# Kernel tuning notes

Measured on AMD Instinct MI355X. Metric: run time of the kernel, lower is better.

Reference implementation:

```python
import jax, jax.numpy as jnp
import numpy as np

EPSILON = 0.1
NUM_ITERS = 50
D = 256


def setup_inputs() -> dict:
    key = jax.random.key(0)
    ks = jax.random.split(key, 12)
    NA, NT = 8192, 8192
    s = 1.0 / np.sqrt(D)
    return {
        "agent_embeddings": jax.random.normal(ks[0], (NA, D), jnp.float32),
        "task_embeddings": jax.random.normal(ks[1], (NT, D), jnp.float32),
        "Wq": jax.random.normal(ks[2], (D, D), jnp.float32) * s,
        "bq": jax.random.normal(ks[3], (D,), jnp.float32) * 0.01,
        "Wk": jax.random.normal(ks[4], (D, D), jnp.float32) * s,
        "bk": jax.random.normal(ks[5], (D,), jnp.float32) * 0.01,
        "W1": jax.random.normal(ks[6], (D, D // 2), jnp.float32) * s,
        "b1": jax.random.normal(ks[7], (D // 2,), jnp.float32) * 0.01,
        "W2": jax.random.normal(ks[8], (D // 2, 1), jnp.float32) * (1.0 / np.sqrt(D // 2)),
        "b2": jax.random.normal(ks[9], (1,), jnp.float32) * 0.01,
    }


def _ot_forward(agent_embeddings, task_embeddings, Wq, bq, Wk, bk, W1, b1, W2, b2):
    num_tasks = task_embeddings.shape[0]
    q = agent_embeddings @ Wq + bq  # [NA, D]
    k = task_embeddings @ Wk + bk   # [NT, D]
    q_norm = jnp.sum(q * q, axis=1, keepdims=True)          # [NA, 1]
    k_norm = jnp.sum(k * k, axis=1, keepdims=True)          # [NT, 1]
    distances = q_norm + k_norm.T - 2.0 * (q @ k.T)          # [NA, NT]
    C = -distances
    supply_logits = (jax.nn.relu(agent_embeddings @ W1 + b1) @ W2 + b2)[:, 0]
    b = jax.nn.softmax(supply_logits, axis=0)                # [NA]
    a = jnp.ones((num_tasks,), dtype=C.dtype) / num_tasks    # [NT]

    log_b = jnp.log(b + 1e-20)
    log_a = jnp.log(a + 1e-20)
    log_K = -C / EPSILON                                     # [NA, NT]

    def body(_, fg):
        f, g = fg
        f = log_b - jax.nn.logsumexp(log_K + g[None, :], axis=1)
        g = log_a - jax.nn.logsumexp(log_K + f[:, None], axis=0)
        return (f, g)

    f0 = jnp.zeros_like(b)
    g0 = jnp.zeros_like(a)
    f, g = jax.lax.fori_loop(0, NUM_ITERS, body, (f0, g0))

    T = jnp.exp(f[:, None] + log_K + g[None, :])
    T = jnp.maximum(T, 0.0)
    T = T / (jnp.sum(T) + 1e-08)
    return T


def reference(agent_embeddings, task_embeddings, Wq, bq, Wk, bk, W1, b1, W2, b2):
    return _ot_forward(agent_embeddings, task_embeddings, Wq, bq, Wk, bk, W1, b1, W2, b2)
```

## Files before the change

### kernel.cpp

```cpp
#include <hip/hip_runtime.h>
#include <math.h>

#define NR 8192
#define DIM 256
#define NBLK 512
#define CROWS 16
#define RSC 2
#define NSUB 8
#define SCALE2 14.426950408889634f

typedef unsigned short ushort_t;
typedef __attribute__((ext_vector_type(8))) short bfrag;
typedef __attribute__((ext_vector_type(4))) float facc;

__device__ __forceinline__ float fexp2(float x) {
#if __has_builtin(__builtin_amdgcn_exp2f)
    return __builtin_amdgcn_exp2f(x);
#else
    return exp2f(x);
#endif
}
__device__ __forceinline__ float flog2(float x) {
#if __has_builtin(__builtin_amdgcn_logf)
    return __builtin_amdgcn_logf(x);
#else
    return log2f(x);
#endif
}

__device__ __forceinline__ void gl2lds16(const float* gp, float* lp) {
#if __has_builtin(__builtin_amdgcn_global_load_lds)
    __builtin_amdgcn_global_load_lds(
        (const __attribute__((address_space(1))) unsigned int*)gp,
        (__attribute__((address_space(3))) unsigned int*)lp, 16, 0, 0);
#else
    *(float4*)lp = *(const float4*)gp;
#endif
}

__device__ __forceinline__ void wait_vm0()  { asm volatile("s_waitcnt vmcnt(0)" ::: "memory"); }
__device__ __forceinline__ void bar_lgkm()  { asm volatile("s_waitcnt lgkmcnt(0)\ns_barrier" ::: "memory"); }

__device__ __forceinline__ void lse_comb2(float& m, float& s, float mo, float so) {
    float nm = fmaxf(m, mo);
    s = s * fexp2(m - nm) + so * fexp2(mo - nm);
    m = nm;
}

__device__ __forceinline__ void lse_upd4(float& m, float& s,
                                         float v0, float v1, float v2, float v3) {
    float m4 = fmaxf(fmaxf(v0, v1), fmaxf(v2, v3));
    float nm = fmaxf(m, m4);
    float e = fexp2(v0 - nm) + fexp2(v1 - nm) + fexp2(v2 - nm) + fexp2(v3 - nm);
    s = fmaf(s, fexp2(m - nm), e);
    m = nm;
}

__device__ __forceinline__ void lse_upd2(float& m, float& s, float v0, float v1) {
    float m2 = fmaxf(v0, v1);
    float nm = fmaxf(m, m2);
    float e = fexp2(v0 - nm) + fexp2(v1 - nm);
    s = fmaf(s, fexp2(m - nm), e);
    m = nm;
}

__device__ __forceinline__ ushort_t f2bf(float x) {
    unsigned u = __float_as_uint(x);
    u += 0x7FFFu + ((u >> 16) & 1u);
    return (ushort_t)(u >> 16);
}
__device__ __forceinline__ float bf2f(ushort_t b) {
    return __uint_as_float(((unsigned)b) << 16);
}

__global__ void init_zero(float* __restrict__ g) {
    int t = blockIdx.x * 256 + threadIdx.x;
    if (t < NR) g[t] = 0.0f;
}

__global__ __launch_bounds__(256) void gemm_qk2(const float* __restrict__ A0,
                                                const float* __restrict__ W0,
                                                const float* __restrict__ bias0,
                                                float* __restrict__ out0,
                                                const float* __restrict__ A1,
                                                const float* __restrict__ W1,
                                                const float* __restrict__ bias1,
                                                float* __restrict__ out1) {
    const float* A    = blockIdx.z ? A1 : A0;
    const float* W    = blockIdx.z ? W1 : W0;
    const float* bias = blockIdx.z ? bias1 : bias0;
    float* out        = blockIdx.z ? out1 : out0;
    __shared__ float As[16][68];
    __shared__ float Ws[16][68];
    const int t  = threadIdx.x;
    const int r0 = blockIdx.x * 64;
    const int c0 = blockIdx.y * 64;
    const int ty = t >> 4, tx = t & 15;
    const int arow = t >> 2;
    const int ak   = (t & 3) * 4;
    const int wrow = t >> 4;
    const int wcol = (t & 15) * 4;
    float acc[4][4] = {};
    for (int k0 = 0; k0 < DIM; k0 += 16) {
        float4 av = *(const float4*)(A + (size_t)(r0 + arow) * DIM + k0 + ak);
        float4 wv = *(const float4*)(W + (size_t)(k0 + wrow) * DIM + c0 + wcol);
        __syncthreads();
        As[ak + 0][arow] = av.x; As[ak + 1][arow] = av.y;
        As[ak + 2][arow] = av.z; As[ak + 3][arow] = av.w;
        *(float4*)&Ws[wrow][wcol] = wv;
        __syncthreads();
#pragma unroll
        for (int kk = 0; kk < 16; ++kk) {
            float4 a = *(const float4*)&As[kk][ty * 4];
            float4 b = *(const float4*)&Ws[kk][tx * 4];
            float aa[4] = {a.x, a.y, a.z, a.w};
            float bb[4] = {b.x, b.y, b.z, b.w};
#pragma unroll
            for (int i = 0; i < 4; ++i)
#pragma unroll
                for (int j = 0; j < 4; ++j)
                    acc[i][j] = fmaf(aa[i], bb[j], acc[i][j]);
        }
    }
#pragma unroll
    for (int i = 0; i < 4; ++i) {
        float4 o;
        o.x = acc[i][0] + bias[c0 + tx * 4 + 0];
        o.y = acc[i][1] + bias[c0 + tx * 4 + 1];
        o.z = acc[i][2] + bias[c0 + tx * 4 + 2];
        o.w = acc[i][3] + bias[c0 + tx * 4 + 3];
        *(float4*)(out + (size_t)(r0 + ty * 4 + i) * DIM + c0 + tx * 4) = o;
    }
}

__global__ __launch_bounds__(64) void row_norm2(const float* __restrict__ q,
                                                float* __restrict__ qn,
                                                const float* __restrict__ k,
                                                float* __restrict__ kn) {
    const int sel = blockIdx.x >> 13;
    const int row = blockIdx.x & (NR - 1);
    const int lane = threadIdx.x;
    const float* x = sel ? k : q;
    float* out     = sel ? kn : qn;
    float4 v = *(const float4*)(x + (size_t)row * DIM + lane * 4);
    float s = v.x * v.x + v.y * v.y + v.z * v.z + v.w * v.w;
#pragma unroll
    for (int off = 32; off > 0; off >>= 1) s += __shfl_xor(s, off);
    if (lane == 0) out[row] = s;
}

__global__ __launch_bounds__(256) void split_bf16_2(const float* __restrict__ q,
                                                    ushort_t* __restrict__ qh,
                                                    ushort_t* __restrict__ ql,
                                                    const float* __restrict__ k,
                                                    ushort_t* __restrict__ kh,
                                                    ushort_t* __restrict__ kl) {
    const int sel = blockIdx.x >> 11;
    const int b = blockIdx.x & 2047;
    const float* x = sel ? k : q;
    ushort_t* hi   = sel ? kh : qh;
    ushort_t* lo   = sel ? kl : ql;
    const int idx = (b * 256 + threadIdx.x) * 4;
    float4 v = *(const float4*)(x + idx);
    ushort_t h0 = f2bf(v.x), h1 = f2bf(v.y), h2 = f2bf(v.z), h3 = f2bf(v.w);
    ushort4 hv = make_ushort4(h0, h1, h2, h3);
    ushort4 lv = make_ushort4(f2bf(v.x - bf2f(h0)), f2bf(v.y - bf2f(h1)),
                              f2bf(v.z - bf2f(h2)), f2bf(v.w - bf2f(h3)));
    *(ushort4*)(hi + idx) = hv;
    *(ushort4*)(lo + idx) = lv;
}

__global__ __launch_bounds__(256) void dist_mfma(const ushort_t* __restrict__ qh,
                                                 const ushort_t* __restrict__ ql,
                                                 const ushort_t* __restrict__ kh,
                                                 const ushort_t* __restrict__ kl,
                                                 const float* __restrict__ qn,
                                                 const float* __restrict__ kn,
                                                 float* __restrict__ S) {
    const int t = threadIdx.x;
    const int wv = t >> 6, lane = t & 63;
    const int r0 = blockIdx.y * 128 + (wv >> 1) * 64;
    const int c0 = blockIdx.x * 128 + (wv & 1) * 64;
    const int fr = lane & 15;
    const int fq = lane >> 4;
    facc acc[4][4];
#pragma unroll
    for (int i = 0; i < 4; ++i)
#pragma unroll
        for (int j = 0; j < 4; ++j) acc[i][j] = (facc){0.f, 0.f, 0.f, 0.f};

    for (int k0 = 0; k0 < DIM; k0 += 32) {
        const int ks = k0 + fq * 8;
        bfrag ah[4], al[4], bh[4], bl[4];
#pragma unroll
        for (int mi = 0; mi < 4; ++mi) {
            const size_t ao = (size_t)(r0 + mi * 16 + fr) * DIM + ks;
            ah[mi] = *(const bfrag*)(qh + ao);
            al[mi] = *(const bfrag*)(ql + ao);
        }
#pragma unroll
        for (int ni = 0; ni < 4; ++ni) {
            const size_t bo = (size_t)(c0 + ni * 16 + fr) * DIM + ks;
            bh[ni] = *(const bfrag*)(kh + bo);
            bl[ni] = *(const bfrag*)(kl + bo);
        }
#pragma unroll
        for (int mi = 0; mi < 4; ++mi)
#pragma unroll
            for (int ni = 0; ni < 4; ++ni) {
                acc[mi][ni] = __builtin_amdgcn_mfma_f32_16x16x32_bf16(ah[mi], bh[ni], acc[mi][ni], 0, 0, 0);
                acc[mi][ni] = __builtin_amdgcn_mfma_f32_16x16x32_bf16(ah[mi], bl[ni], acc[mi][ni], 0, 0, 0);
                acc[mi][ni] = __builtin_amdgcn_mfma_f32_16x16x32_bf16(al[mi], bh[ni], acc[mi][ni], 0, 0, 0);
                acc[mi][ni] = __builtin_amdgcn_mfma_f32_16x16x32_bf16(al[mi], bl[ni], acc[mi][ni], 0, 0, 0);
            }
    }
#pragma unroll
    for (int mi = 0; mi < 4; ++mi) {
        float qnr[4];
#pragma unroll
        for (int r = 0; r < 4; ++r) qnr[r] = qn[r0 + mi * 16 + fq * 4 + r];
#pragma unroll
        for (int ni = 0; ni < 4; ++ni) {
            const int col = c0 + ni * 16 + fr;
            const float knc = kn[col];
#pragma unroll
            for (int r = 0; r < 4; ++r) {
                const int row = r0 + mi * 16 + fq * 4 + r;
                S[(size_t)row * NR + col] = (qnr[r] + knc - 2.0f * acc[mi][ni][r]) * SCALE2;
            }
        }
    }
}

__global__ __launch_bounds__(128) void mlp_logits(const float* __restrict__ A,
                                                  const float* __restrict__ W1,
                                                  const float* __restrict__ b1,
                                                  const float* __restrict__ W2,
                                                  const float* __restrict__ b2,
                                                  float* __restrict__ logits) {
    __shared__ float ar[DIM];
    __shared__ float red[2];
    const int t = threadIdx.x;
    const int row = blockIdx.x;
    *(float2*)&ar[t * 2] = *(const float2*)(A + (size_t)row * DIM + t * 2);
    __syncthreads();
    float h = b1[t];
#pragma unroll 8
    for (int kk = 0; kk < DIM; ++kk) h = fmaf(ar[kk], W1[kk * 128 + t], h);
    float val = fmaxf(h, 0.0f) * W2[t];
#pragma unroll
    for (int off = 32; off > 0; off >>= 1) val += __shfl_xor(val, off);
    if ((t & 63) == 0) red[t >> 6] = val;
    __syncthreads();
    if (t == 0) logits[row] = red[0] + red[1] + b2[0];
}

__global__ __launch_bounds__(1024) void softmax_logb(const float* __restrict__ logits,
                                                     float* __restrict__ logb2) {
    __shared__ float redm[16], reds[16];
    const int t = threadIdx.x;
    float l[8];
    float m = -INFINITY;
#pragma unroll
    for (int i = 0; i < 8; ++i) { l[i] = logits[i * 1024 + t]; m = fmaxf(m, l[i]); }
#pragma unroll
    for (int off = 32; off > 0; off >>= 1) m = fmaxf(m, __shfl_xor(m, off));
    if ((t & 63) == 0) redm[t >> 6] = m;
    __syncthreads();
    if (t < 64) {
        float v = (t < 16) ? redm[t] : -INFINITY;
#pragma unroll
        for (int off = 8; off > 0; off >>= 1) v = fmaxf(v, __shfl_xor(v, off));
        if (t == 0) redm[0] = v;
    }
    __syncthreads();
    m = redm[0];
    float s = 0.0f;
#pragma unroll
    for (int i = 0; i < 8; ++i) s += __expf(l[i] - m);
#pragma unroll
    for (int off = 32; off > 0; off >>= 1) s += __shfl_xor(s, off);
    if ((t & 63) == 0) reds[t >> 6] = s;
    __syncthreads();
    if (t < 64) {
        float v = (t < 16) ? reds[t] : 0.0f;
#pragma unroll
        for (int off = 8; off > 0; off >>= 1) v += __shfl_xor(v, off);
        if (t == 0) reds[0] = v;
    }
    __syncthreads();
    s = reds[0];
    float invs = 1.0f / s;
#pragma unroll
    for (int i = 0; i < 8; ++i)
        logb2[i * 1024 + t] = log2f(__expf(l[i] - m) * invs + 1e-20f);
}

__global__ __launch_bounds__(512, 4) void iter_fused(const float* __restrict__ S,
                                                     const float* __restrict__ g,
                                                     const float* __restrict__ logb2,
                                                     float* __restrict__ f,
                                                     float* __restrict__ pm) {
    __shared__ float buf[RSC][NR];
    __shared__ float redm[8], reds[8];
    const int t = threadIdx.x;
    const int wv = t >> 6, lane = t & 63;
    const int chunk = blockIdx.x;
    const int r0 = chunk * CROWS;
    const int rw = wv >> 2;
    const int qt = wv & 3;
    const int qbase = qt * 2048;
    const int loff = lane * 4;

    float4 greg[8];
#pragma unroll
    for (int it = 0; it < 8; ++it)
        greg[it] = *(const float4*)(g + qbase + it * 256 + loff);

    float cm[4][4], cs[4][4];
#pragma unroll
    for (int j = 0; j < 4; ++j)
#pragma unroll
        for (int c = 0; c < 4; ++c) { cm[j][c] = -INFINITY; cs[j][c] = 0.0f; }

    {
        const float* Sr = S + (size_t)(r0 + rw) * NR + qbase;
        float* ld = &buf[rw][qbase];
#pragma unroll
        for (int it = 0; it < 8; ++it)
#if __has_builtin(__builtin_amdgcn_global_load_lds)
            gl2lds16(Sr + it * 256 + loff, ld + it * 256);
#else
            gl2lds16(Sr + it * 256 + loff, ld + it * 256 + loff);
#endif
    }

    for (int sc = 0; sc < NSUB; ++sc) {
        wait_vm0();
        float m = -INFINITY, s = 0.0f;
#pragma unroll
        for (int it = 0; it < 8; ++it) {
            float4 v = *(const float4*)&buf[rw][qbase + it * 256 + loff];
            float4 gv = greg[it];
            lse_upd4(m, s, v.x + gv.x, v.y + gv.y, v.z + gv.z, v.w + gv.w);
        }
#pragma unroll
        for (int off = 32; off > 0; off >>= 1) {
            float mo = __shfl_xor(m, off);
            float so = __shfl_xor(s, off);
            lse_comb2(m, s, mo, so);
        }
        if (lane == 0) { redm[wv] = m; reds[wv] = s; }
        bar_lgkm();

        float fr[RSC];
#pragma unroll
        for (int r = 0; r < RSC; ++r) {
            float mm = redm[r * 4 + 0], ss = reds[r * 4 + 0];
            lse_comb2(mm, ss, redm[r * 4 + 1], reds[r * 4 + 1]);
            lse_comb2(mm, ss, redm[r * 4 + 2], reds[r * 4 + 2]);
            lse_comb2(mm, ss, redm[r * 4 + 3], reds[r * 4 + 3]);
            fr[r] = logb2[r0 + sc * RSC + r] - (mm + flog2(ss));
        }
        if (t < RSC) f[r0 + sc * RSC + t] = fr[t];

#pragma unroll
        for (int j = 0; j < 4; ++j) {
            const int c = j * 2048 + t * 4;
            float4 a = *(const float4*)&buf[0][c];
            float4 bb = *(const float4*)&buf[1][c];
            lse_upd2(cm[j][0], cs[j][0], a.x + fr[0], bb.x + fr[1]);
            lse_upd2(cm[j][1], cs[j][1], a.y + fr[0], bb.y + fr[1]);
            lse_upd2(cm[j][2], cs[j][2], a.z + fr[0], bb.z + fr[1]);
            lse_upd2(cm[j][3], cs[j][3], a.w + fr[0], bb.w + fr[1]);
        }
        bar_lgkm();

        if (sc + 1 < NSUB) {
            const float* Sn = S + (size_t)(r0 + (sc + 1) * RSC + rw) * NR + qbase;
            float* ld = &buf[rw][qbase];
#pragma unroll
            for (int it = 0; it < 8; ++it)
#if __has_builtin(__builtin_amdgcn_global_load_lds)
                gl2lds16(Sn + it * 256 + loff, ld + it * 256);
#else
                gl2lds16(Sn + it * 256 + loff, ld + it * 256 + loff);
#endif
        }
    }
#pragma unroll
    for (int j = 0; j < 4; ++j) {
        float4 L;
        L.x = cm[j][0] + flog2(cs[j][0]);
        L.y = cm[j][1] + flog2(cs[j][1]);
        L.z = cm[j][2] + flog2(cs[j][2]);
        L.w = cm[j][3] + flog2(cs[j][3]);
        *(float4*)&pm[(size_t)chunk * NR + j * 2048 + t * 4] = L;
    }
}

__global__ __launch_bounds__(1024) void col_combine(const float* __restrict__ pm,
                                                    float* __restrict__ g,
                                                    float log_a2) {
    __shared__ float Lm[32][32], Ls[32][32];
    __shared__ float Lm2[8][32], Ls2[8][32];
    const int t = threadIdx.x;
    const int cl = t & 31;
    const int grp = t >> 5;
    const int col = blockIdx.x * 32 + cl;
    float m = -INFINITY, s = 0.0f;
#pragma unroll
    for (int i = 0; i < 16; i += 4) {
        float l0 = pm[(size_t)(grp * 16 + i + 0) * NR + col];
        float l1 = pm[(size_t)(grp * 16 + i + 1) * NR + col];
        float l2 = pm[(size_t)(grp * 16 + i + 2) * NR + col];
        float l3 = pm[(size_t)(grp * 16 + i + 3) * NR + col];
        lse_upd4(m, s, l0, l1, l2, l3);
    }
    Lm[grp][cl] = m; Ls[grp][cl] = s;
    __syncthreads();
    if (t < 256) {
        const int c = t & 31, q = t >> 5;
        float mm = Lm[q * 4 + 0][c], ss = Ls[q * 4 + 0][c];
        lse_comb2(mm, ss, Lm[q * 4 + 1][c], Ls[q * 4 + 1][c]);
        lse_comb2(mm, ss, Lm[q * 4 + 2][c], Ls[q * 4 + 2][c]);
        lse_comb2(mm, ss, Lm[q * 4 + 3][c], Ls[q * 4 + 3][c]);
        Lm2[q][c] = mm; Ls2[q][c] = ss;
    }
    __syncthreads();
    if (t < 32) {
        float mm = Lm2[0][t], ss = Ls2[0][t];
#pragma unroll
        for (int q = 1; q < 8; ++q) lse_comb2(mm, ss, Lm2[q][t], Ls2[q][t]);
        g[blockIdx.x * 32 + t] = log_a2 - (mm + flog2(ss));
    }
}

__global__ __launch_bounds__(256) void write_pass(const float* S,
                                                  const float* __restrict__ f,
                                                  const float* __restrict__ g,
                                                  float* out) {
    const int wv = threadIdx.x >> 6, lane = threadIdx.x & 63;
    const int row = blockIdx.x * 4 + wv;
    const float fi = f[row];
    const float4* Sr = (const float4*)(S + (size_t)row * NR);
    const float4* gr = (const float4*)g;
    float4* Or = (float4*)(out + (size_t)row * NR);
#pragma unroll 4
    for (int it = 0; it < NR / 256; ++it) {
        const int idx = it * 64 + lane;
        float4 sv = Sr[idx];
        float4 gv = gr[idx];
        float4 o;
        o.x = fexp2(fi + sv.x + gv.x);
        o.y = fexp2(fi + sv.y + gv.y);
        o.z = fexp2(fi + sv.z + gv.z);
        o.w = fexp2(fi + sv.w + gv.w);
        Or[idx] = o;
    }
}

extern "C" void kernel_launch(void* const* d_in, const int* in_sizes, int n_in,
                              void* d_out, int out_size, void* d_ws, size_t ws_size,
                              hipStream_t stream) {
    (void)in_sizes; (void)n_in; (void)out_size; (void)ws_size;
    const float* A  = (const float*)d_in[0];
    const float* Tk = (const float*)d_in[1];
    const float* Wq = (const float*)d_in[2];
    const float* bq = (const float*)d_in[3];
    const float* Wk = (const float*)d_in[4];
    const float* bk = (const float*)d_in[5];
    const float* W1 = (const float*)d_in[6];
    const float* b1 = (const float*)d_in[7];
    const float* W2 = (const float*)d_in[8];
    const float* b2 = (const float*)d_in[9];
    float* S  = (float*)d_out;
    float* ws = (float*)d_ws;
    float* qn     = ws; ws += NR;
    float* kn     = ws; ws += NR;
    float* logb2  = ws; ws += NR;
    float* logits = ws; ws += NR;
    float* f      = ws; ws += NR;
    float* g      = ws; ws += NR;
    float* pm     = ws; ws += (size_t)NBLK * NR;
    float* q      = ws; ws += (size_t)NR * DIM;
    float* k      = ws; ws += (size_t)NR * DIM;
    ushort_t* qh = (ushort_t*)pm;
    ushort_t* ql = qh + (size_t)NR * DIM;
    ushort_t* kh = ql + (size_t)NR * DIM;
    ushort_t* kl = kh + (size_t)NR * DIM;

    const float log_a2 = -13.0f;

    init_zero<<<32, 256, 0, stream>>>(g);
    gemm_qk2<<<dim3(128, 4, 2), 256, 0, stream>>>(A, Wq, bq, q, Tk, Wk, bk, k);
    row_norm2<<<2 * NR, 64, 0, stream>>>(q, qn, k, kn);
    split_bf16_2<<<2 * (NR * DIM / 1024), 256, 0, stream>>>(q, qh, ql, k, kh, kl);
    mlp_logits<<<NR, 128, 0, stream>>>(A, W1, b1, W2, b2, logits);
    softmax_logb<<<1, 1024, 0, stream>>>(logits, logb2);
    dist_mfma<<<dim3(64, 64), 256, 0, stream>>>(qh, ql, kh, kl, qn, kn, S);
    for (int it = 0; it < 50; ++it) {
        iter_fused<<<NBLK, 512, 0, stream>>>(S, g, logb2, f, pm);
        col_combine<<<NR / 32, 1024, 0, stream>>>(pm, g, log_a2);
    }
    write_pass<<<NR / 4, 256, 0, stream>>>(S, f, g, S);
}
```

Baseline: 3.422 ms.

## Stage distance GEMM operands through swizzled LDS tiles shared across waves

The bf16-split distance GEMM previously had every wave load its A/B fragments directly from global memory, so operands were reloaded redundantly across waves. Each wave now copies one of the four hi/lo operand tiles into LDS with direct global-to-LDS loads, using an XOR swizzle to avoid bank conflicts. Fragments are then read from LDS in a staged order that keeps register pressure low, and launch bounds request three blocks per CU. The loop is not double-buffered, so each k-step adds two barriers and a full wait on global loads.

```diff
diff --git a/kernel.cpp b/kernel.cpp
--- a/kernel.cpp
+++ b/kernel.cpp
@@ -8,6 +8,7 @@
 #define RSC 2
 #define NSUB 8
 #define SCALE2 14.426950408889634f
+#define SW3(r) ((((r) >> 2) ^ (r)) & 3)
 
 typedef unsigned short ushort_t;
 typedef __attribute__((ext_vector_type(8))) short bfrag;
@@ -29,6 +30,15 @@
 }
 
 __device__ __forceinline__ void gl2lds16(const float* gp, float* lp) {
+#if __has_builtin(__builtin_amdgcn_global_load_lds)
+    __builtin_amdgcn_global_load_lds(
+        (const __attribute__((address_space(1))) unsigned int*)gp,
+        (__attribute__((address_space(3))) unsigned int*)lp, 16, 0, 0);
+#else
+    *(float4*)lp = *(const float4*)gp;
+#endif
+}
+__device__ __forceinline__ void gl2lds16u(const ushort_t* gp, ushort_t* lp) {
 #if __has_builtin(__builtin_amdgcn_global_load_lds)
     __builtin_amdgcn_global_load_lds(
         (const __attribute__((address_space(1))) unsigned int*)gp,
@@ -170,19 +180,29 @@
     *(ushort4*)(lo + idx) = lv;
 }
 
-__global__ __launch_bounds__(256) void dist_mfma(const ushort_t* __restrict__ qh,
-                                                 const ushort_t* __restrict__ ql,
-                                                 const ushort_t* __restrict__ kh,
-                                                 const ushort_t* __restrict__ kl,
-                                                 const float* __restrict__ qn,
-                                                 const float* __restrict__ kn,
-                                                 float* __restrict__ S) {
+__global__ __launch_bounds__(256, 3) void dist_mfma(const ushort_t* __restrict__ qh,
+                                                    const ushort_t* __restrict__ ql,
+                                                    const ushort_t* __restrict__ kh,
+                                                    const ushort_t* __restrict__ kl,
+                                                    const float* __restrict__ qn,
+                                                    const float* __restrict__ kn,
+                                                    float* __restrict__ S) {
+    __shared__ ushort_t Ah[128 * 32], Al[128 * 32], Bh[128 * 32], Bl[128 * 32];
     const int t = threadIdx.x;
     const int wv = t >> 6, lane = t & 63;
-    const int r0 = blockIdx.y * 128 + (wv >> 1) * 64;
-    const int c0 = blockIdx.x * 128 + (wv & 1) * 64;
+    const int r0 = blockIdx.y * 128;
+    const int c0 = blockIdx.x * 128;
     const int fr = lane & 15;
     const int fq = lane >> 4;
+    const int arow = (wv >> 1) * 64;
+    const int brow = (wv & 1) * 64;
+
+    const ushort_t* gsrc = (wv == 0) ? qh : (wv == 1) ? ql : (wv == 2) ? kh : kl;
+    ushort_t* ltile      = (wv == 0) ? Ah : (wv == 1) ? Al : (wv == 2) ? Bh : Bl;
+    const int gbase = (wv < 2) ? r0 : c0;
+    const int prow = lane >> 2;
+    const int pchunk = lane & 3;
+
     facc acc[4][4];
 #pragma unroll
     for (int i = 0; i < 4; ++i)
@@ -190,42 +210,76 @@
         for (int j = 0; j < 4; ++j) acc[i][j] = (facc){0.f, 0.f, 0.f, 0.f};
 
     for (int k0 = 0; k0 < DIM; k0 += 32) {
-        const int ks = k0 + fq * 8;
-        bfrag ah[4], al[4], bh[4], bl[4];
+#pragma unroll
+        for (int i = 0; i < 8; ++i) {
+            const int row = i * 16 + prow;
+            const int lchunk = pchunk ^ SW3(row);
+            const ushort_t* sp = gsrc + (size_t)(gbase + row) * DIM + k0 + lchunk * 8;
+#if __has_builtin(__builtin_amdgcn_global_load_lds)
+            gl2lds16u(sp, ltile + i * 512);
+#else
+            gl2lds16u(sp, ltile + i * 512 + lane * 8);
+#endif
+        }
+        wait_vm0();
+        __syncthreads();
+
+        bfrag fa[4], fb[4], f2[4];
 #pragma unroll
         for (int mi = 0; mi < 4; ++mi) {
-            const size_t ao = (size_t)(r0 + mi * 16 + fr) * DIM + ks;
-            ah[mi] = *(const bfrag*)(qh + ao);
-            al[mi] = *(const bfrag*)(ql + ao);
+            const int ar = arow + mi * 16 + fr;
+            fa[mi] = *(const bfrag*)(Ah + ar * 32 + (fq ^ SW3(ar)) * 8);
         }
 #pragma unroll
         for (int ni = 0; ni < 4; ++ni) {
-            const size_t bo = (size_t)(c0 + ni * 16 + fr) * DIM + ks;
-            bh[ni] = *(const bfrag*)(kh + bo);
-            bl[ni] = *(const bfrag*)(kl + bo);
+            const int br = brow + ni * 16 + fr;
+            fb[ni] = *(const bfrag*)(Bh + br * 32 + (fq ^ SW3(br)) * 8);
         }
 #pragma unroll
         for (int mi = 0; mi < 4; ++mi)
 #pragma unroll
-            for (int ni = 0; ni < 4; ++ni) {
-                acc[mi][ni] = __builtin_amdgcn_mfma_f32_16x16x32_bf16(ah[mi], bh[ni], acc[mi][ni], 0, 0, 0);
-                acc[mi][ni] = __builtin_amdgcn_mfma_f32_16x16x32_bf16(ah[mi], bl[ni], acc[mi][ni], 0, 0, 0);
-                acc[mi][ni] = __builtin_amdgcn_mfma_f32_16x16x32_bf16(al[mi], bh[ni], acc[mi][ni], 0, 0, 0);
-                acc[mi][ni] = __builtin_amdgcn_mfma_f32_16x16x32_bf16(al[mi], bl[ni], acc[mi][ni], 0, 0, 0);
-            }
+            for (int ni = 0; ni < 4; ++ni)
+                acc[mi][ni] = __builtin_amdgcn_mfma_f32_16x16x32_bf16(fa[mi], fb[ni], acc[mi][ni], 0, 0, 0);
+#pragma unroll
+        for (int mi = 0; mi < 4; ++mi) {
+            const int ar = arow + mi * 16 + fr;
+            f2[mi] = *(const bfrag*)(Al + ar * 32 + (fq ^ SW3(ar)) * 8);
+        }
+#pragma unroll
+        for (int mi = 0; mi < 4; ++mi)
+#pragma unroll
+            for (int ni = 0; ni < 4; ++ni)
+                acc[mi][ni] = __builtin_amdgcn_mfma_f32_16x16x32_bf16(f2[mi], fb[ni], acc[mi][ni], 0, 0, 0);
+#pragma unroll
+        for (int ni = 0; ni < 4; ++ni) {
+            const int br = brow + ni * 16 + fr;
+            fb[ni] = *(const bfrag*)(Bl + br * 32 + (fq ^ SW3(br)) * 8);
+        }
+#pragma unroll
+        for (int mi = 0; mi < 4; ++mi)
+#pragma unroll
+            for (int ni = 0; ni < 4; ++ni)
+                acc[mi][ni] = __builtin_amdgcn_mfma_f32_16x16x32_bf16(fa[mi], fb[ni], acc[mi][ni], 0, 0, 0);
+#pragma unroll
+        for (int mi = 0; mi < 4; ++mi)
+#pragma unroll
+            for (int ni = 0; ni < 4; ++ni)
+                acc[mi][ni] = __builtin_amdgcn_mfma_f32_16x16x32_bf16(f2[mi], fb[ni], acc[mi][ni], 0, 0, 0);
+
+        __syncthreads();
     }
 #pragma unroll
     for (int mi = 0; mi < 4; ++mi) {
         float qnr[4];
 #pragma unroll
-        for (int r = 0; r < 4; ++r) qnr[r] = qn[r0 + mi * 16 + fq * 4 + r];
+        for (int r = 0; r < 4; ++r) qnr[r] = qn[r0 + arow + mi * 16 + fq * 4 + r];
 #pragma unroll
         for (int ni = 0; ni < 4; ++ni) {
-            const int col = c0 + ni * 16 + fr;
+            const int col = c0 + brow + ni * 16 + fr;
             const float knc = kn[col];
 #pragma unroll
             for (int r = 0; r < 4; ++r) {
-                const int row = r0 + mi * 16 + fq * 4 + r;
+                const int row = r0 + arow + mi * 16 + fq * 4 + r;
                 S[(size_t)row * NR + col] = (qnr[r] + knc - 2.0f * acc[mi][ni][r]) * SCALE2;
             }
         }
```

Measured after the change: 3.334 ms. 1.03x faster.
